# Performance work log

Hardware: AMD Instinct MI355X
Metric: run time of the kernel (lower is better)

Reference implementation:

```python
import jax, jax.numpy as jnp
import numpy as np

BN_EPS = 1e-5

def _bn(x, gamma, beta):
    # training-mode BatchNorm1d: batch statistics over dim 0 (biased var)
    m = x.mean(0)
    v = x.var(0)
    return (x - m) * jax.lax.rsqrt(v + BN_EPS) * gamma + beta

def _lstm_cell(h, c, xt, Wih, Whh, b):
    # PyTorch gate order: i, f, g, o
    g = xt @ Wih.T + h @ Whh.T + b
    i, f, gg, o = jnp.split(g, 4, axis=-1)
    c = jax.nn.sigmoid(f) * c + jax.nn.sigmoid(i) * jnp.tanh(gg)
    h = jax.nn.sigmoid(o) * jnp.tanh(c)
    return h, c


def setup_inputs() -> dict:
    key = jax.random.key(0)
    ks = jax.random.split(key, 12)
    V, E, H = 10000, 512, 1024
    D = 2 * H
    B, S = 32, 256
    s_e = 1.0 / np.sqrt(E)
    s_h = 1.0 / np.sqrt(H)
    s_d = 1.0 / np.sqrt(D)
    return {
        "x": jax.random.randint(ks[0], (B, S), 0, V, dtype=jnp.int32),
        "emb": jax.random.normal(ks[1], (V, E), jnp.float32),
        "Wih_f": jax.random.normal(ks[2], (4 * H, E), jnp.float32) * s_e,
        "Whh_f": jax.random.normal(ks[3], (4 * H, H), jnp.float32) * s_h,
        "b_f": jnp.zeros((4 * H,), jnp.float32),
        "Wih_b": jax.random.normal(ks[4], (4 * H, E), jnp.float32) * s_e,
        "Whh_b": jax.random.normal(ks[5], (4 * H, H), jnp.float32) * s_h,
        "b_b": jnp.zeros((4 * H,), jnp.float32),
        "Wih_d": jax.random.normal(ks[6], (4 * D, E), jnp.float32) * s_e,
        "Whh_d": jax.random.normal(ks[7], (4 * D, D), jnp.float32) * s_d,
        "b_d": jnp.zeros((4 * D,), jnp.float32),
        "enc_gamma": jnp.ones((D,), jnp.float32),
        "enc_beta": jnp.zeros((D,), jnp.float32),
        "dec_gamma": jnp.ones((D,), jnp.float32),
        "dec_beta": jnp.zeros((D,), jnp.float32),
        "fcW": jax.random.normal(ks[8], (V, D), jnp.float32) * s_d,
        "fcb": jnp.zeros((V,), jnp.float32),
    }


def reference(x, emb, Wih_f, Whh_f, b_f, Wih_b, Whh_b, b_b,
              Wih_d, Whh_d, b_d, enc_gamma, enc_beta,
              dec_gamma, dec_beta, fcW, fcb):
    B, S = x.shape
    H = Whh_f.shape[1]
    V = fcW.shape[0]
    xe = emb[x]                      # [B, S, E]
    xs = jnp.swapaxes(xe, 0, 1)      # [S, B, E]
    z = jnp.zeros((B, H), xe.dtype)

    def enc_fwd(carry, xt):
        h, c = _lstm_cell(carry[0], carry[1], xt, Wih_f, Whh_f, b_f)
        return (h, c), None

    def enc_bwd(carry, xt):
        h, c = _lstm_cell(carry[0], carry[1], xt, Wih_b, Whh_b, b_b)
        return (h, c), None

    (hf, _), _ = jax.lax.scan(enc_fwd, (z, z), xs)
    (hb, _), _ = jax.lax.scan(enc_bwd, (z, z), xs[::-1])

    hn = jnp.concatenate([hf, hb], axis=-1)          # [B, 2H]
    hn = jax.nn.relu(_bn(hn, enc_gamma, enc_beta))   # dropout = identity (eval)

    def dec_step(carry, _):
        h, c, tok = carry
        xt = emb[tok]                                # [B, E]
        h, c = _lstm_cell(h, c, xt, Wih_d, Whh_d, b_d)
        out = jax.nn.relu(_bn(h, dec_gamma, dec_beta))
        logits = out @ fcW.T + fcb                   # [B, V]
        tok = jnp.argmax(logits, axis=-1)
        return (h, c, tok), logits

    init = (hn, jnp.zeros_like(hn), x[:, 0])
    _, logits_seq = jax.lax.scan(dec_step, init, None, length=S - 1)  # [S-1, B, V]

    outputs = jnp.concatenate(
        [jnp.zeros((B, 1, V), xe.dtype), jnp.swapaxes(logits_seq, 0, 1)], axis=1)
    return outputs
```

## Files before the change

### kernel.cpp

```cpp
#include <hip/hip_runtime.h>
#include <math.h>

#define BB 32
#define SS 256
#define EE 512
#define HH 1024
#define DD 2048
#define VV 10000

typedef __attribute__((ext_vector_type(8))) short short8v;
typedef __attribute__((ext_vector_type(4))) float f32x4;

typedef unsigned short ushort_t;
typedef unsigned long long u64;


__device__ __forceinline__ ushort_t f2bf(float f) {
  unsigned u = __float_as_uint(f);
  return (ushort_t)((u + 0x7FFFu + ((u >> 16) & 1u)) >> 16);
}
__device__ __forceinline__ float bf2f(ushort_t h) {
  return __uint_as_float(((unsigned)h) << 16);
}
__device__ __forceinline__ unsigned enc_f32(float f) {
  unsigned u = __float_as_uint(f);
  return (u & 0x80000000u) ? ~u : (u | 0x80000000u);
}
__device__ __forceinline__ float sigm(float v) { return 1.0f / (1.0f + expf(-v)); }

union Frag { short8v v; ushort_t u[8]; };

__global__ __launch_bounds__(256) void k_pack_wdec(const float* __restrict__ Whh,
                                                   const float* __restrict__ Wih,
                                                   ushort_t* __restrict__ Wp) {
  int i = blockIdx.x * 256 + threadIdx.x;
  int lane = i & 63, nt = (i >> 6) & 511, fpkt = i >> 15;
  int rho = nt * 16 + (lane & 15);
  int blk = rho >> 5, idx = rho & 31, g = idx >> 3, c = idx & 7;
  int n = g * DD + blk * 8 + c;
  int k0 = fpkt * 32 + (lane >> 4) * 8;
  const float* src = (k0 < DD) ? (Whh + (size_t)n * DD + k0)
                               : (Wih + (size_t)n * EE + (k0 - DD));
  size_t ohi = ((((size_t)fpkt * 2 + 0) * 512 + nt) * 64 + lane) * 8;
  size_t olo = ((((size_t)fpkt * 2 + 1) * 512 + nt) * 64 + lane) * 8;
#pragma unroll
  for (int e = 0; e < 8; ++e) {
    float v = src[e];
    ushort_t hi = f2bf(v);
    Wp[ohi + e] = hi;
    Wp[olo + e] = f2bf(v - bf2f(hi));
  }
}

__global__ __launch_bounds__(256) void k_pack_wfc(const float* __restrict__ fcW,
                                                  ushort_t* __restrict__ Wp) {
  int i = blockIdx.x * 256 + threadIdx.x;
  int lane = i & 63, nt = (i >> 6) % 626, fpkt = i / (626 * 64);
  int rho = nt * 16 + (lane & 15);
  int n = rho < VV ? rho : VV - 1;
  int k0 = fpkt * 32 + (lane >> 4) * 8;
  const float* src = fcW + (size_t)n * DD + k0;
  size_t ohi = ((((size_t)fpkt * 2 + 0) * 626 + nt) * 64 + lane) * 8;
  size_t olo = ((((size_t)fpkt * 2 + 1) * 626 + nt) * 64 + lane) * 8;
#pragma unroll
  for (int e = 0; e < 8; ++e) {
    float v = src[e];
    ushort_t hi = f2bf(v);
    Wp[ohi + e] = hi;
    Wp[olo + e] = f2bf(v - bf2f(hi));
  }
}

__global__ __launch_bounds__(256) void k_pack_wenc(
    const float* __restrict__ Whh_f, const float* __restrict__ Wih_f,
    const float* __restrict__ Whh_b, const float* __restrict__ Wih_b,
    ushort_t* __restrict__ Wp) {
  int i = blockIdx.x * 256 + threadIdx.x;
  int lane = i & 63, nt = (i >> 6) & 511, fpkt = i >> 15;
  int rho = nt * 16 + (lane & 15);
  int blk = rho >> 5, idx = rho & 31, g = idx >> 3, c = idx & 7;
  int dir = blk >> 7;
  int r = g * HH + (blk & 127) * 8 + c;
  const float* Whh = dir ? Whh_b : Whh_f;
  const float* Wih = dir ? Wih_b : Wih_f;
  int k0 = fpkt * 32 + (lane >> 4) * 8;
  const float* src = (k0 < HH) ? (Whh + (size_t)r * HH + k0)
                               : (Wih + (size_t)r * EE + (k0 - HH));
  size_t ohi = ((((size_t)fpkt * 2 + 0) * 512 + nt) * 64 + lane) * 8;
  size_t olo = ((((size_t)fpkt * 2 + 1) * 512 + nt) * 64 + lane) * 8;
#pragma unroll
  for (int e = 0; e < 8; ++e) {
    float v = src[e];
    ushort_t hi = f2bf(v);
    Wp[ohi + e] = hi;
    Wp[olo + e] = f2bf(v - bf2f(hi));
  }
}

__global__ __launch_bounds__(256) void k_zero32(unsigned* __restrict__ p, int n) {
  int i = blockIdx.x * 256 + threadIdx.x;
  if (i < n) p[i] = 0u;
}
__global__ __launch_bounds__(256) void k_out0(float* __restrict__ out) {
  int i = blockIdx.x * 256 + threadIdx.x;
  if (i < BB * VV) out[(size_t)(i / VV) * SS * VV + (i % VV)] = 0.0f;
}

__device__ __forceinline__ void pack_act(ushort_t* __restrict__ dst, int j, int b,
                                         float v) {
  int fpkt = j >> 5, kloc = j & 31;
  int lane = (kloc >> 3) * 16 + (b & 15);
  int e = kloc & 7, mt = b >> 4;
  ushort_t hi = f2bf(v);
  dst[((((size_t)fpkt * 2 + 0) * 2 + mt) * 64 + lane) * 8 + e] = hi;
  dst[((((size_t)fpkt * 2 + 1) * 2 + mt) * 64 + lane) * 8 + e] = f2bf(v - bf2f(hi));
}

__device__ __forceinline__ void split8(const float* __restrict__ src, Frag& fh,
                                       Frag& fl) {
  float4 v0 = *(const float4*)src;
  float4 v1 = *(const float4*)(src + 4);
  float vv[8] = {v0.x, v0.y, v0.z, v0.w, v1.x, v1.y, v1.z, v1.w};
#pragma unroll
  for (int e = 0; e < 8; ++e) {
    ushort_t hi = f2bf(vv[e]);
    fh.u[e] = hi;
    fl.u[e] = f2bf(vv[e] - bf2f(hi));
  }
}

__global__ __launch_bounds__(512) void k_enc_mfma(
    int t, const int* __restrict__ x, const float* __restrict__ emb,
    const ushort_t* __restrict__ Wp, ushort_t* __restrict__ hencp,
    float* __restrict__ cT2, float* __restrict__ hT2,
    const float* __restrict__ b_f, const float* __restrict__ b_b) {
  __shared__ float red[8 * 2 * 2 * 64 * 4];
  __shared__ int stoks[32];
  const int tid = threadIdx.x, w = tid >> 6, lane = tid & 63;
  const int dir = blockIdx.x >> 7, jb = (blockIdx.x & 127) * 8;
  const int s = dir ? (SS - 1 - t) : t;
  const int pin = t & 1;
  const size_t HEP = 32 * 2 * 2 * 64 * 8;
  const ushort_t* hin = hencp + (dir * 2 + pin) * HEP;
  ushort_t* hout = hencp + (dir * 2 + (pin ^ 1)) * HEP;
  if (tid < 32) stoks[tid] = x[tid * SS + s];
  __syncthreads();

  f32x4 acc[2][2];
#pragma unroll
  for (int a = 0; a < 2; ++a)
#pragma unroll
    for (int bq = 0; bq < 2; ++bq) acc[a][bq] = (f32x4){0.f, 0.f, 0.f, 0.f};

  for (int i = 0; i < 6; ++i) {
    const int kt = w + 8 * i;
    Frag ah[2], al[2], wh[2], wl[2];
    if (kt < 32) {
#pragma unroll
      for (int mt = 0; mt < 2; ++mt) {
        ah[mt].v = *(const short8v*)(hin + ((((size_t)kt * 2 + 0) * 2 + mt) * 64 + lane) * 8);
        al[mt].v = *(const short8v*)(hin + ((((size_t)kt * 2 + 1) * 2 + mt) * 64 + lane) * 8);
      }
    } else {
      const int ke = (kt - 32) * 32 + (lane >> 4) * 8;
#pragma unroll
      for (int mt = 0; mt < 2; ++mt) {
        const int b = mt * 16 + (lane & 15);
        split8(emb + (size_t)stoks[b] * EE + ke, ah[mt], al[mt]);
      }
    }
#pragma unroll
    for (int nt = 0; nt < 2; ++nt) {
      const size_t ntg = blockIdx.x * 2 + nt;
      wh[nt].v = *(const short8v*)(Wp + ((((size_t)kt * 2 + 0) * 512 + ntg) * 64 + lane) * 8);
      wl[nt].v = *(const short8v*)(Wp + ((((size_t)kt * 2 + 1) * 512 + ntg) * 64 + lane) * 8);
    }
#pragma unroll
    for (int mt = 0; mt < 2; ++mt)
#pragma unroll
      for (int nt = 0; nt < 2; ++nt) {
        acc[mt][nt] = __builtin_amdgcn_mfma_f32_16x16x32_bf16(ah[mt].v, wh[nt].v, acc[mt][nt], 0, 0, 0);
        acc[mt][nt] = __builtin_amdgcn_mfma_f32_16x16x32_bf16(ah[mt].v, wl[nt].v, acc[mt][nt], 0, 0, 0);
        acc[mt][nt] = __builtin_amdgcn_mfma_f32_16x16x32_bf16(al[mt].v, wh[nt].v, acc[mt][nt], 0, 0, 0);
      }
  }
#pragma unroll
  for (int mt = 0; mt < 2; ++mt)
#pragma unroll
    for (int nt = 0; nt < 2; ++nt)
      ((f32x4*)red)[((w * 2 + mt) * 2 + nt) * 64 + lane] = acc[mt][nt];
  __syncthreads();

  if (tid < 256) {
    const int c = tid >> 5, b = tid & 31;
    const float* bias = dir ? b_b : b_f;
    const int mt = b >> 4, lg = (b & 15) >> 2, reg = b & 3;
    float g4[4];
#pragma unroll
    for (int g = 0; g < 4; ++g) {
      const int rho = g * 8 + c;
      const int nt = rho >> 4, l15 = rho & 15;
      float v = bias[g * HH + jb + c];
#pragma unroll
      for (int w2 = 0; w2 < 8; ++w2)
        v += red[(((w2 * 2 + mt) * 2 + nt) * 64 + lg * 16 + l15) * 4 + reg];
      g4[g] = v;
    }
    const int j = jb + c;
    float* cT = cT2 + dir * (HH * BB);
    float* hT = hT2 + dir * (HH * BB);
    const int idx = j * BB + b;
    float cv = fmaf(sigm(g4[1]), cT[idx], sigm(g4[0]) * tanhf(g4[2]));
    cT[idx] = cv;
    float h = sigm(g4[3]) * tanhf(cv);
    hT[idx] = h;
    pack_act(hout, j, b, h);
  }
}

__global__ __launch_bounds__(256) void k_bn_handoff(
    const float* __restrict__ hT2, const float* __restrict__ gamma,
    const float* __restrict__ beta, ushort_t* __restrict__ hdp) {
  const int d = blockIdx.x * 8 + (threadIdx.x >> 5);
  const int b = threadIdx.x & 31;
  float v = hT2[(d < HH ? d * BB : (HH * BB) + (d - HH) * BB) + b];
  float sum = v;
  for (int m = 16; m >= 1; m >>= 1) sum += __shfl_xor(sum, m, 32);
  float mean = sum * (1.0f / BB);
  float dx = v - mean;
  float s2 = dx * dx;
  for (int m = 16; m >= 1; m >>= 1) s2 += __shfl_xor(s2, m, 32);
  float var = s2 * (1.0f / BB);
  float y = fmaxf(dx * (1.0f / sqrtf(var + 1e-5f)) * gamma[d] + beta[d], 0.0f);
  pack_act(hdp, d, b, y);
}

__global__ __launch_bounds__(512) void k_dec_mfma(
    int t, const int* __restrict__ x, const float* __restrict__ emb,
    const ushort_t* __restrict__ Wp, ushort_t* __restrict__ hdp,
    float* __restrict__ cdT, ushort_t* __restrict__ outp,
    const float* __restrict__ bias, const float* __restrict__ gamma,
    const float* __restrict__ beta, const u64* __restrict__ winners) {
  __shared__ float red[8 * 2 * 2 * 64 * 4];
  __shared__ int stoks[32];
  const int tid = threadIdx.x, w = tid >> 6, lane = tid & 63;
  const int jb = blockIdx.x * 8;
  const int pin = t & 1;
  const size_t HDP = 64 * 2 * 2 * 64 * 8;
  const ushort_t* hin = hdp + pin * HDP;
  ushort_t* hout = hdp + (pin ^ 1) * HDP;
  if (tid < 32)
    stoks[tid] = (t == 0) ? x[tid * SS]
                          : (int)(0xFFFFFFFFu -
                                  (unsigned)(winners[((t - 1) & 1) * 32 + tid] & 0xFFFFFFFFull));
  __syncthreads();

  f32x4 acc[2][2];
#pragma unroll
  for (int a = 0; a < 2; ++a)
#pragma unroll
    for (int bq = 0; bq < 2; ++bq) acc[a][bq] = (f32x4){0.f, 0.f, 0.f, 0.f};

  for (int i = 0; i < 10; ++i) {
    const int kt = w + 8 * i;
    Frag ah[2], al[2], wh[2], wl[2];
    if (kt < 64) {
#pragma unroll
      for (int mt = 0; mt < 2; ++mt) {
        ah[mt].v = *(const short8v*)(hin + ((((size_t)kt * 2 + 0) * 2 + mt) * 64 + lane) * 8);
        al[mt].v = *(const short8v*)(hin + ((((size_t)kt * 2 + 1) * 2 + mt) * 64 + lane) * 8);
      }
    } else {
      const int ke = (kt - 64) * 32 + (lane >> 4) * 8;
#pragma unroll
      for (int mt = 0; mt < 2; ++mt) {
        const int b = mt * 16 + (lane & 15);
        split8(emb + (size_t)stoks[b] * EE + ke, ah[mt], al[mt]);
      }
    }
#pragma unroll
    for (int nt = 0; nt < 2; ++nt) {
      const size_t ntg = blockIdx.x * 2 + nt;
      wh[nt].v = *(const short8v*)(Wp + ((((size_t)kt * 2 + 0) * 512 + ntg) * 64 + lane) * 8);
      wl[nt].v = *(const short8v*)(Wp + ((((size_t)kt * 2 + 1) * 512 + ntg) * 64 + lane) * 8);
    }
#pragma unroll
    for (int mt = 0; mt < 2; ++mt)
#pragma unroll
      for (int nt = 0; nt < 2; ++nt) {
        acc[mt][nt] = __builtin_amdgcn_mfma_f32_16x16x32_bf16(ah[mt].v, wh[nt].v, acc[mt][nt], 0, 0, 0);
        acc[mt][nt] = __builtin_amdgcn_mfma_f32_16x16x32_bf16(ah[mt].v, wl[nt].v, acc[mt][nt], 0, 0, 0);
        acc[mt][nt] = __builtin_amdgcn_mfma_f32_16x16x32_bf16(al[mt].v, wh[nt].v, acc[mt][nt], 0, 0, 0);
      }
  }
#pragma unroll
  for (int mt = 0; mt < 2; ++mt)
#pragma unroll
    for (int nt = 0; nt < 2; ++nt)
      ((f32x4*)red)[((w * 2 + mt) * 2 + nt) * 64 + lane] = acc[mt][nt];
  __syncthreads();

  if (tid < 256) {
    const int c = tid >> 5, b = tid & 31;
    const int mt = b >> 4, lg = (b & 15) >> 2, reg = b & 3;
    float g4[4];
#pragma unroll
    for (int g = 0; g < 4; ++g) {
      const int rho = g * 8 + c;
      const int nt = rho >> 4, l15 = rho & 15;
      float v = bias[g * DD + jb + c];
#pragma unroll
      for (int w2 = 0; w2 < 8; ++w2)
        v += red[(((w2 * 2 + mt) * 2 + nt) * 64 + lg * 16 + l15) * 4 + reg];
      g4[g] = v;
    }
    const int j = jb + c;
    const int idx = j * BB + b;
    float cv = fmaf(sigm(g4[1]), cdT[idx], sigm(g4[0]) * tanhf(g4[2]));
    cdT[idx] = cv;
    float h = sigm(g4[3]) * tanhf(cv);
    pack_act(hout, j, b, h);
    float sum = h;
    for (int m = 16; m >= 1; m >>= 1) sum += __shfl_xor(sum, m, 32);
    float mean = sum * (1.0f / BB);
    float dx = h - mean;
    float s2v = dx * dx;
    for (int m = 16; m >= 1; m >>= 1) s2v += __shfl_xor(s2v, m, 32);
    float var = s2v * (1.0f / BB);
    float y = fmaxf(dx * (1.0f / sqrtf(var + 1e-5f)) * gamma[j] + beta[j], 0.0f);
    pack_act(outp, j, b, y);
  }
}

__global__ __launch_bounds__(512) void k_fc_mfma(
    int t, const ushort_t* __restrict__ outp, const ushort_t* __restrict__ Wp,
    const float* __restrict__ fcb, float* __restrict__ out,
    u64* __restrict__ winners) {
  __shared__ float red[8 * 2 * 2 * 64 * 4];
  __shared__ u64 kred[16][32];
  const int tid = threadIdx.x, w = tid >> 6, lane = tid & 63;

  f32x4 acc[2][2];
#pragma unroll
  for (int a = 0; a < 2; ++a)
#pragma unroll
    for (int bq = 0; bq < 2; ++bq) acc[a][bq] = (f32x4){0.f, 0.f, 0.f, 0.f};

  for (int i = 0; i < 8; ++i) {
    const int kt = w + 8 * i;
    Frag ah[2], al[2], wh[2], wl[2];
#pragma unroll
    for (int mt = 0; mt < 2; ++mt) {
      ah[mt].v = *(const short8v*)(outp + ((((size_t)kt * 2 + 0) * 2 + mt) * 64 + lane) * 8);
      al[mt].v = *(const short8v*)(outp + ((((size_t)kt * 2 + 1) * 2 + mt) * 64 + lane) * 8);
    }
#pragma unroll
    for (int nt = 0; nt < 2; ++nt) {
      const size_t ntg = blockIdx.x * 2 + nt;
      wh[nt].v = *(const short8v*)(Wp + ((((size_t)kt * 2 + 0) * 626 + ntg) * 64 + lane) * 8);
      wl[nt].v = *(const short8v*)(Wp + ((((size_t)kt * 2 + 1) * 626 + ntg) * 64 + lane) * 8);
    }
#pragma unroll
    for (int mt = 0; mt < 2; ++mt)
#pragma unroll
      for (int nt = 0; nt < 2; ++nt) {
        acc[mt][nt] = __builtin_amdgcn_mfma_f32_16x16x32_bf16(ah[mt].v, wh[nt].v, acc[mt][nt], 0, 0, 0);
        acc[mt][nt] = __builtin_amdgcn_mfma_f32_16x16x32_bf16(ah[mt].v, wl[nt].v, acc[mt][nt], 0, 0, 0);
        acc[mt][nt] = __builtin_amdgcn_mfma_f32_16x16x32_bf16(al[mt].v, wh[nt].v, acc[mt][nt], 0, 0, 0);
      }
  }
#pragma unroll
  for (int mt = 0; mt < 2; ++mt)
#pragma unroll
    for (int nt = 0; nt < 2; ++nt)
      ((f32x4*)red)[((w * 2 + mt) * 2 + nt) * 64 + lane] = acc[mt][nt];
  __syncthreads();

  {
    const int r2 = tid >> 5, b = tid & 31;
    const int mt = b >> 4, lg = (b & 15) >> 2, reg = b & 3;
    const size_t obase = (size_t)b * SS * VV + (size_t)(t + 1) * VV;
    u64 bestkey = 0ull;
#pragma unroll
    for (int q = 0; q < 2; ++q) {
      const int rho = r2 * 2 + q;
      const int v = blockIdx.x * 32 + rho;
      if (v < VV) {
        const int nt = rho >> 4, l15 = rho & 15;
        float val = fcb[v];
#pragma unroll
        for (int w2 = 0; w2 < 8; ++w2)
          val += red[(((w2 * 2 + mt) * 2 + nt) * 64 + lg * 16 + l15) * 4 + reg];
        out[obase + v] = val;
        u64 key = ((u64)enc_f32(val) << 32) | (0xFFFFFFFFu - (unsigned)v);
        if (key > bestkey) bestkey = key;
      }
    }
    kred[r2][b] = bestkey;
  }
  __syncthreads();
#pragma unroll
  for (int m = 8; m >= 1; m >>= 1) {
    if ((tid >> 5) < m) {
      u64 o = kred[(tid >> 5) + m][tid & 31];
      if (o > kred[tid >> 5][tid & 31]) kred[tid >> 5][tid & 31] = o;
    }
    __syncthreads();
  }
  if ((tid >> 5) == 0) atomicMax(&winners[(t & 1) * 32 + (tid & 31)], kred[0][tid & 31]);
  if (blockIdx.x == 0 && (tid >> 5) == 1) winners[((t + 1) & 1) * 32 + (tid & 31)] = 0ull;
}

#define DOT4A(acc, q, r)                                                      \
  acc = fmaf((q).x, (r).x, acc); acc = fmaf((q).y, (r).y, acc);               \
  acc = fmaf((q).z, (r).z, acc); acc = fmaf((q).w, (r).w, acc);
__device__ __forceinline__ int colof(int b) { return (b & 3) * 8 + (b >> 2); }

__global__ __launch_bounds__(256) void k_zero_v7(float* __restrict__ p, int n) {
  int i = blockIdx.x * 256 + threadIdx.x;
  if (i < n) p[i] = 0.0f;
}
__global__ __launch_bounds__(256) void k_out0_v7(float* __restrict__ out,
                                                 u64* __restrict__ winners) {
  int i = blockIdx.x * 256 + threadIdx.x;
  if (i < BB * VV) out[(size_t)(i / VV) * SS * VV + (i % VV)] = 0.0f;
  if (i < 64) winners[i] = 0ull;
}
__global__ __launch_bounds__(256) void k_embed_v7(const int* __restrict__ x,
                                                  const float* __restrict__ emb,
                                                  float* __restrict__ xeT) {
  int i = blockIdx.x * 256 + threadIdx.x;
  int c = i & 3, col = (i >> 2) & 31, k4 = (i >> 7) & 127, s = i >> 14;
  int b = (col & 7) * 4 + (col >> 3);
  xeT[i] = emb[(size_t)x[b * SS + s] * EE + (k4 * 4 + c)];
}
__global__ __launch_bounds__(512, 2) void k_enc_step_v7(
    int t, const float* __restrict__ xeT, float* __restrict__ hfT,
    float* __restrict__ cfT, float* __restrict__ hbT, float* __restrict__ cbT,
    const float* __restrict__ Wih_f, const float* __restrict__ Whh_f,
    const float* __restrict__ b_f, const float* __restrict__ Wih_b,
    const float* __restrict__ Whh_b, const float* __restrict__ b_b) {
  __shared__ float wlds[2][32 * 33 * 4];
  __shared__ float alds[2][1024 * 4];
  const int tid = threadIdx.x;
  const int rg = tid & 7, bg = (tid >> 3) & 7, s = tid >> 6;
  const int dir = blockIdx.x >> 7, jb = (blockIdx.x & 127) * 8;
  const float* __restrict__ Wih = dir ? Wih_b : Wih_f;
  const float* __restrict__ Whh = dir ? Whh_b : Whh_f;
  const float* __restrict__ bias = dir ? b_b : b_f;
  float* hT = dir ? hbT : hfT;
  float* cT = dir ? cbT : cfT;
  const int sstep = dir ? (SS - 1 - t) : t;
  const int pin = t & 1;
  const float4* __restrict__ hin4 = (const float4*)(hT + pin * (HH * BB));
  const float4* __restrict__ xs4 = (const float4*)(xeT + (size_t)sstep * EE * BB);
  float* __restrict__ hout = hT + (pin ^ 1) * (HH * BB);
  const int NC = 12;
  auto wsrc = [&](int cc, int idx) -> float4 {
    int lrow = idx >> 5, k4 = idx & 31;
    int grow = (lrow >> 3) * HH + jb + (lrow & 7);
    return (cc < 8) ? ((const float4*)(Whh + (size_t)grow * HH))[cc * 32 + k4]
                    : ((const float4*)(Wih + (size_t)grow * EE))[(cc - 8) * 32 + k4];
  };
  auto asrc = [&](int cc, int idx) -> float4 {
    return (cc < 8) ? hin4[cc * 1024 + idx] : xs4[(cc - 8) * 1024 + idx];
  };
  auto wdst = [&](int buf, int idx) -> float4* {
    return (float4*)&wlds[buf][((idx >> 5) * 33 + (idx & 31)) * 4];
  };
  {
    float4 w0 = wsrc(0, tid), w1 = wsrc(0, 512 + tid);
    float4 a0 = asrc(0, tid), a1 = asrc(0, 512 + tid);
    *wdst(0, tid) = w0; *wdst(0, 512 + tid) = w1;
    ((float4*)alds[0])[tid] = a0; ((float4*)alds[0])[512 + tid] = a1;
  }
  __syncthreads();
  float acc[4][4];
#pragma unroll
  for (int i = 0; i < 4; ++i)
#pragma unroll
    for (int j = 0; j < 4; ++j) acc[i][j] = 0.0f;
  for (int cc = 0; cc < NC; ++cc) {
    const int cb = cc & 1;
    float4 pw0, pw1, pa0, pa1;
    const bool pref = (cc + 1 < NC);
    if (pref) {
      pw0 = wsrc(cc + 1, tid); pw1 = wsrc(cc + 1, 512 + tid);
      pa0 = asrc(cc + 1, tid); pa1 = asrc(cc + 1, 512 + tid);
    }
    const float4* __restrict__ ap = (const float4*)alds[cb];
    const float4* __restrict__ wp = (const float4*)wlds[cb];
#pragma unroll
    for (int sub = 0; sub < 4; ++sub) {
      const int k4 = sub * 8 + s;
      float4 av[4], wv[4];
#pragma unroll
      for (int j = 0; j < 4; ++j) av[j] = ap[k4 * 32 + j * 8 + bg];
#pragma unroll
      for (int i = 0; i < 4; ++i) wv[i] = wp[(rg + 8 * i) * 33 + k4];
#pragma unroll
      for (int i = 0; i < 4; ++i)
#pragma unroll
        for (int j = 0; j < 4; ++j) { DOT4A(acc[i][j], wv[i], av[j]); }
    }
    if (pref) {
      *wdst(cb ^ 1, tid) = pw0; *wdst(cb ^ 1, 512 + tid) = pw1;
      ((float4*)alds[cb ^ 1])[tid] = pa0; ((float4*)alds[cb ^ 1])[512 + tid] = pa1;
    }
    __syncthreads();
  }
  float* red = &wlds[0][0];
#pragma unroll
  for (int i = 0; i < 4; ++i)
#pragma unroll
    for (int j = 0; j < 4; ++j)
      red[(s * 32 + (rg + 8 * i)) * 32 + (bg * 4 + j)] = acc[i][j];
  __syncthreads();
  if (tid < 256) {
    const int c = tid >> 5, b = tid & 31;
    float g4[4];
#pragma unroll
    for (int g = 0; g < 4; ++g) {
      float v = bias[g * HH + jb + c];
#pragma unroll
      for (int s2 = 0; s2 < 8; ++s2) v += red[(s2 * 32 + g * 8 + c) * 32 + b];
      g4[g] = v;
    }
    const int j = jb + c;
    const int idx = j * BB + b;
    float cv = fmaf(sigm(g4[1]), cT[idx], sigm(g4[0]) * tanhf(g4[2]));
    cT[idx] = cv;
    hout[(j >> 2) * 128 + colof(b) * 4 + (j & 3)] = sigm(g4[3]) * tanhf(cv);
  }
}
__global__ __launch_bounds__(256) void k_enc_bn_v7(
    const float* __restrict__ hfT, const float* __restrict__ hbT,
    const float* __restrict__ gamma, const float* __restrict__ beta,
    float* __restrict__ hdT) {
  const int d = blockIdx.x * 8 + (threadIdx.x >> 5);
  const int b = threadIdx.x & 31;
  const int dl = (d < HH) ? d : d - HH;
  const float* __restrict__ src = (d < HH) ? hfT : hbT;
  float v = src[(dl >> 2) * 128 + colof(b) * 4 + (dl & 3)];
  float sum = v;
  for (int m = 16; m >= 1; m >>= 1) sum += __shfl_xor(sum, m, 32);
  float mean = sum * (1.0f / BB);
  float dx = v - mean;
  float s2 = dx * dx;
  for (int m = 16; m >= 1; m >>= 1) s2 += __shfl_xor(s2, m, 32);
  float var = s2 * (1.0f / BB);
  float y = dx * (1.0f / sqrtf(var + 1e-5f)) * gamma[d] + beta[d];
  hdT[(d >> 2) * 128 + colof(b) * 4 + (d & 3)] = fmaxf(y, 0.0f);
}
__global__ __launch_bounds__(512, 2) void k_dec_gates_v7(
    int t, const int* __restrict__ x, const float* __restrict__ emb,
    float* __restrict__ hdT, float* __restrict__ cdT, float* __restrict__ outT,
    const float* __restrict__ Wih, const float* __restrict__ Whh,
    const float* __restrict__ bias, const float* __restrict__ gamma,
    const float* __restrict__ beta, const u64* __restrict__ winners) {
  __shared__ float wlds[2][32 * 33 * 4];
  __shared__ float alds[2][1024 * 4];
  __shared__ int stoks[32];
  const int tid = threadIdx.x;
  const int rg = tid & 7, bg = (tid >> 3) & 7, s = tid >> 6;
  const int jb = blockIdx.x * 8;
  const int pin = t & 1;
  const float4* __restrict__ hin4 = (const float4*)(hdT + pin * (DD * BB));
  float* __restrict__ hout = hdT + (pin ^ 1) * (DD * BB);
  if (tid < 32)
    stoks[tid] = (t == 0) ? x[tid * SS]
                          : (int)(0xFFFFFFFFu -
                                  (unsigned)(winners[((t - 1) & 1) * 32 + tid] & 0xFFFFFFFFull));
  const int NC = 20;
  auto wsrc = [&](int cc, int idx) -> float4 {
    int lrow = idx >> 5, k4 = idx & 31;
    int grow = (lrow >> 3) * DD + jb + (lrow & 7);
    return (cc < 16) ? ((const float4*)(Whh + (size_t)grow * DD))[cc * 32 + k4]
                     : ((const float4*)(Wih + (size_t)grow * EE))[(cc - 16) * 32 + k4];
  };
  auto asrc = [&](int cc, int idx) -> float4 {
    if (cc < 16) return hin4[cc * 1024 + idx];
    int col = idx & 31;
    int b = (col & 7) * 4 + (col >> 3);
    return ((const float4*)(emb + (size_t)stoks[b] * EE))[(cc - 16) * 32 + (idx >> 5)];
  };
  auto wdst = [&](int buf, int idx) -> float4* {
    return (float4*)&wlds[buf][((idx >> 5) * 33 + (idx & 31)) * 4];
  };
  {
    float4 w0 = wsrc(0, tid), w1 = wsrc(0, 512 + tid);
    float4 a0 = asrc(0, tid), a1 = asrc(0, 512 + tid);
    *wdst(0, tid) = w0; *wdst(0, 512 + tid) = w1;
    ((float4*)alds[0])[tid] = a0; ((float4*)alds[0])[512 + tid] = a1;
  }
  __syncthreads();
  float acc[4][4];
#pragma unroll
  for (int i = 0; i < 4; ++i)
#pragma unroll
    for (int j = 0; j < 4; ++j) acc[i][j] = 0.0f;
  for (int cc = 0; cc < NC; ++cc) {
    const int cb = cc & 1;
    float4 pw0, pw1, pa0, pa1;
    const bool pref = (cc + 1 < NC);
    if (pref) {
      pw0 = wsrc(cc + 1, tid); pw1 = wsrc(cc + 1, 512 + tid);
      pa0 = asrc(cc + 1, tid); pa1 = asrc(cc + 1, 512 + tid);
    }
    const float4* __restrict__ ap = (const float4*)alds[cb];
    const float4* __restrict__ wp = (const float4*)wlds[cb];
#pragma unroll
    for (int sub = 0; sub < 4; ++sub) {
      const int k4 = sub * 8 + s;
      float4 av[4], wv[4];
#pragma unroll
      for (int j = 0; j < 4; ++j) av[j] = ap[k4 * 32 + j * 8 + bg];
#pragma unroll
      for (int i = 0; i < 4; ++i) wv[i] = wp[(rg + 8 * i) * 33 + k4];
#pragma unroll
      for (int i = 0; i < 4; ++i)
#pragma unroll
        for (int j = 0; j < 4; ++j) { DOT4A(acc[i][j], wv[i], av[j]); }
    }
    if (pref) {
      *wdst(cb ^ 1, tid) = pw0; *wdst(cb ^ 1, 512 + tid) = pw1;
      ((float4*)alds[cb ^ 1])[tid] = pa0; ((float4*)alds[cb ^ 1])[512 + tid] = pa1;
    }
    __syncthreads();
  }
  float* red = &wlds[0][0];
#pragma unroll
  for (int i = 0; i < 4; ++i)
#pragma unroll
    for (int j = 0; j < 4; ++j)
      red[(s * 32 + (rg + 8 * i)) * 32 + (bg * 4 + j)] = acc[i][j];
  __syncthreads();
  if (tid < 256) {
    const int c = tid >> 5, b = tid & 31;
    float g4[4];
#pragma unroll
    for (int g = 0; g < 4; ++g) {
      float v = bias[g * DD + jb + c];
#pragma unroll
      for (int s2 = 0; s2 < 8; ++s2) v += red[(s2 * 32 + g * 8 + c) * 32 + b];
      g4[g] = v;
    }
    const int j = jb + c;
    const int idx = j * BB + b;
    float cv = fmaf(sigm(g4[1]), cdT[idx], sigm(g4[0]) * tanhf(g4[2]));
    cdT[idx] = cv;
    float h = sigm(g4[3]) * tanhf(cv);
    hout[(j >> 2) * 128 + colof(b) * 4 + (j & 3)] = h;
    float sum = h;
    for (int m = 16; m >= 1; m >>= 1) sum += __shfl_xor(sum, m, 32);
    float mean = sum * (1.0f / BB);
    float dx = h - mean;
    float s2v = dx * dx;
    for (int m = 16; m >= 1; m >>= 1) s2v += __shfl_xor(s2v, m, 32);
    float var = s2v * (1.0f / BB);
    float y = dx * (1.0f / sqrtf(var + 1e-5f)) * gamma[j] + beta[j];
    outT[(j >> 2) * 128 + colof(b) * 4 + (j & 3)] = fmaxf(y, 0.0f);
  }
}
__global__ __launch_bounds__(512, 2) void k_fc_v7(
    int t, const float* __restrict__ outT, const float* __restrict__ fcW,
    const float* __restrict__ fcb, float* __restrict__ out,
    u64* __restrict__ winners) {
  __shared__ float wlds[2][40 * 33 * 4];
  __shared__ float alds[2][1024 * 4];
  __shared__ u64 kred[16][32];
  const int tid = threadIdx.x;
  const int rg = tid & 7, bg = (tid >> 3) & 7, s = tid >> 6;
  const int vb = blockIdx.x * 40;
  const float4* __restrict__ xa4 = (const float4*)outT;
  const int NC = 16;
  auto wsrc = [&](int cc, int idx) -> float4 {
    int lrow = idx >> 5, k4 = idx & 31;
    return ((const float4*)(fcW + (size_t)(vb + lrow) * DD))[cc * 32 + k4];
  };
  auto wdst = [&](int buf, int idx) -> float4* {
    return (float4*)&wlds[buf][((idx >> 5) * 33 + (idx & 31)) * 4];
  };
  {
    float4 w0 = wsrc(0, tid), w1 = wsrc(0, 512 + tid);
    float4 a0 = xa4[tid], a1 = xa4[512 + tid];
    *wdst(0, tid) = w0; *wdst(0, 512 + tid) = w1;
    if (tid < 256) *wdst(0, 1024 + tid) = wsrc(0, 1024 + tid);
    ((float4*)alds[0])[tid] = a0; ((float4*)alds[0])[512 + tid] = a1;
  }
  __syncthreads();
  float acc[5][4];
#pragma unroll
  for (int i = 0; i < 5; ++i)
#pragma unroll
    for (int j = 0; j < 4; ++j) acc[i][j] = 0.0f;
  for (int cc = 0; cc < NC; ++cc) {
    const int cb = cc & 1;
    float4 pw0, pw1, pw2, pa0, pa1;
    const bool pref = (cc + 1 < NC);
    if (pref) {
      pw0 = wsrc(cc + 1, tid); pw1 = wsrc(cc + 1, 512 + tid);
      if (tid < 256) pw2 = wsrc(cc + 1, 1024 + tid);
      pa0 = xa4[(cc + 1) * 1024 + tid];
      pa1 = xa4[(cc + 1) * 1024 + 512 + tid];
    }
    const float4* __restrict__ ap = (const float4*)alds[cb];
    const float4* __restrict__ wp = (const float4*)wlds[cb];
#pragma unroll
    for (int sub = 0; sub < 4; ++sub) {
      const int k4 = sub * 8 + s;
      float4 av[4], wv[5];
#pragma unroll
      for (int j = 0; j < 4; ++j) av[j] = ap[k4 * 32 + j * 8 + bg];
#pragma unroll
      for (int i = 0; i < 5; ++i) wv[i] = wp[(rg + 8 * i) * 33 + k4];
#pragma unroll
      for (int i = 0; i < 5; ++i)
#pragma unroll
        for (int j = 0; j < 4; ++j) { DOT4A(acc[i][j], wv[i], av[j]); }
    }
    if (pref) {
      *wdst(cb ^ 1, tid) = pw0; *wdst(cb ^ 1, 512 + tid) = pw1;
      if (tid < 256) *wdst(cb ^ 1, 1024 + tid) = pw2;
      ((float4*)alds[cb ^ 1])[tid] = pa0; ((float4*)alds[cb ^ 1])[512 + tid] = pa1;
    }
    __syncthreads();
  }
  float* red = &wlds[0][0];
#pragma unroll
  for (int i = 0; i < 5; ++i)
#pragma unroll
    for (int j = 0; j < 4; ++j)
      red[(s * 40 + (rg + 8 * i)) * 32 + (bg * 4 + j)] = acc[i][j];
  __syncthreads();
  const int r = tid >> 5, b = tid & 31;
  const size_t obase = (size_t)b * SS * VV + (size_t)(t + 1) * VV;
  u64 bestkey = 0ull;
  for (int lrow = r; lrow < 40; lrow += 16) {
    const int v = vb + lrow;
    float val = fcb[v];
#pragma unroll
    for (int s2 = 0; s2 < 8; ++s2) val += red[(s2 * 40 + lrow) * 32 + b];
    out[obase + v] = val;
    u64 key = ((u64)enc_f32(val) << 32) | (0xFFFFFFFFu - (unsigned)v);
    if (key > bestkey) bestkey = key;
  }
  kred[r][b] = bestkey;
  __syncthreads();
#pragma unroll
  for (int m = 8; m >= 1; m >>= 1) {
    if (r < m) {
      u64 o = kred[r + m][b];
      if (o > kred[r][b]) kred[r][b] = o;
    }
    __syncthreads();
  }
  if (r == 0) atomicMax(&winners[(t & 1) * 32 + b], kred[0][b]);
  if (blockIdx.x == 0 && r == 1) winners[((t + 1) & 1) * 32 + b] = 0ull;
}

extern "C" void kernel_launch(void* const* d_in, const int* in_sizes, int n_in,
                              void* d_out, int out_size, void* d_ws, size_t ws_size,
                              hipStream_t stream) {
  const int*   x         = (const int*)d_in[0];
  const float* emb       = (const float*)d_in[1];
  const float* Wih_f     = (const float*)d_in[2];
  const float* Whh_f     = (const float*)d_in[3];
  const float* b_f       = (const float*)d_in[4];
  const float* Wih_b     = (const float*)d_in[5];
  const float* Whh_b     = (const float*)d_in[6];
  const float* b_b       = (const float*)d_in[7];
  const float* Wih_d     = (const float*)d_in[8];
  const float* Whh_d     = (const float*)d_in[9];
  const float* b_d       = (const float*)d_in[10];
  const float* enc_gamma = (const float*)d_in[11];
  const float* enc_beta  = (const float*)d_in[12];
  const float* dec_gamma = (const float*)d_in[13];
  const float* dec_beta  = (const float*)d_in[14];
  const float* fcW       = (const float*)d_in[15];
  const float* fcb       = (const float*)d_in[16];
  float* out = (float*)d_out;

  const size_t WDEC_U = (size_t)80 * 2 * 512 * 512;
  const size_t WFC_U  = (size_t)64 * 2 * 626 * 512;
  const size_t WENC_U = (size_t)48 * 2 * 512 * 512;
  const size_t HDP_U  = (size_t)64 * 2 * 2 * 512;
  const size_t HEP_U  = (size_t)32 * 2 * 2 * 512;
  const size_t need = (WDEC_U + WFC_U + WENC_U + 2 * HDP_U + HDP_U + 4 * HEP_U) * 2 +
                      (size_t)(HH * BB * 2 + DD * BB + HH * BB * 2) * 4 + 512;

  if (ws_size >= need + 1024) {
    ushort_t* us = (ushort_t*)d_ws;
    ushort_t* Wpdec = us;               us += WDEC_U;
    ushort_t* Wpfc  = us;               us += WFC_U;
    ushort_t* Wpenc = us;               us += WENC_U;
    ushort_t* hdp   = us;               us += 2 * HDP_U;
    ushort_t* outp  = us;               us += HDP_U;
    ushort_t* hencp = us;               us += 4 * HEP_U;
    float* f = (float*)us;
    float* cT2  = f;  f += HH * BB * 2;
    float* cdT  = f;  f += DD * BB;
    float* hT2  = f;  f += HH * BB * 2;
    u64* winners = (u64*)f;

    k_pack_wdec<<<10240, 256, 0, stream>>>(Whh_d, Wih_d, Wpdec);
    k_pack_wfc<<<10016, 256, 0, stream>>>(fcW, Wpfc);
    k_pack_wenc<<<6144, 256, 0, stream>>>(Whh_f, Wih_f, Whh_b, Wih_b, Wpenc);
    {
      size_t zbytes = (2 * HDP_U + HDP_U + 4 * HEP_U) * 2 +
                      (size_t)(HH * BB * 2 + DD * BB + HH * BB * 2) * 4 + 512;
      int zn = (int)(zbytes / 4);
      k_zero32<<<(zn + 255) / 256, 256, 0, stream>>>((unsigned*)hdp, zn);
    }
    k_out0<<<(BB * VV + 255) / 256, 256, 0, stream>>>(out);

    for (int t = 0; t < SS; ++t)
      k_enc_mfma<<<256, 512, 0, stream>>>(t, x, emb, Wpenc, hencp, cT2, hT2, b_f, b_b);

    k_bn_handoff<<<DD / 8, 256, 0, stream>>>(hT2, enc_gamma, enc_beta, hdp);

    for (int t = 0; t < SS - 1; ++t) {
      k_dec_mfma<<<256, 512, 0, stream>>>(t, x, emb, Wpdec, hdp, cdT, outp,
                                          b_d, dec_gamma, dec_beta, winners);
      k_fc_mfma<<<313, 512, 0, stream>>>(t, outp, Wpfc, fcb, out, winners);
    }
    return;
  }

  float* ws = (float*)d_ws;
  size_t off = 0;
  float* xeT = ws + off; off += (size_t)SS * EE * BB;
  float* hfT = ws + off; off += 2 * HH * BB;
  float* hbT = ws + off; off += 2 * HH * BB;
  float* cfT = ws + off; off += HH * BB;
  float* cbT = ws + off; off += HH * BB;
  float* hdT = ws + off; off += 2 * DD * BB;
  float* cdT = ws + off; off += DD * BB;
  float* outT = ws + off; off += DD * BB;
  u64* winners = (u64*)(ws + off); off += 128;

  const int nz = 2 * HH * BB * 2 + HH * BB * 2 + 2 * DD * BB + DD * BB;
  k_zero_v7<<<(nz + 255) / 256, 256, 0, stream>>>(hfT, nz);
  k_out0_v7<<<(BB * VV + 255) / 256, 256, 0, stream>>>(out, winners);
  k_embed_v7<<<(SS * EE * BB) / 256, 256, 0, stream>>>(x, emb, xeT);

  for (int t = 0; t < SS; ++t)
    k_enc_step_v7<<<256, 512, 0, stream>>>(t, xeT, hfT, cfT, hbT, cbT,
                                           Wih_f, Whh_f, b_f, Wih_b, Whh_b, b_b);
  k_enc_bn_v7<<<DD / 8, 256, 0, stream>>>(hfT, hbT, enc_gamma, enc_beta, hdT);
  for (int t = 0; t < SS - 1; ++t) {
    k_dec_gates_v7<<<DD / 8, 512, 0, stream>>>(t, x, emb, hdT, cdT, outT,
                                               Wih_d, Whh_d, b_d,
                                               dec_gamma, dec_beta, winners);
    k_fc_v7<<<VV / 40, 512, 0, stream>>>(t, outT, fcW, fcb, out, winners);
  }
}
```

Before: 12.64 ms.

## Use single-bf16 FC weights with exact fp32 rescoring of near-max argmax candidates

The FC projection now stores only the high bf16 part of fcW and drops the lo-weight MFMA pass, with 48 columns per block instead of 32. Argmax moves out of the FC kernel into a new rescue kernel. For each batch row it finds logits within a fixed margin of the max and recomputes those candidates exactly in fp32 from an fp32 copy of the activations, which keeps greedy token choice stable. The logits written to the output now carry the reduced-precision error, and the fallback fp32 path is removed.

```diff
diff --git a/kernel.cpp b/kernel.cpp
--- a/kernel.cpp
+++ b/kernel.cpp
@@ -15,16 +15,14 @@
 typedef unsigned long long u64;
 
 
+#define DELTA 0.125f
+
 __device__ __forceinline__ ushort_t f2bf(float f) {
   unsigned u = __float_as_uint(f);
   return (ushort_t)((u + 0x7FFFu + ((u >> 16) & 1u)) >> 16);
 }
 __device__ __forceinline__ float bf2f(ushort_t h) {
   return __uint_as_float(((unsigned)h) << 16);
-}
-__device__ __forceinline__ unsigned enc_f32(float f) {
-  unsigned u = __float_as_uint(f);
-  return (u & 0x80000000u) ? ~u : (u | 0x80000000u);
 }
 __device__ __forceinline__ float sigm(float v) { return 1.0f / (1.0f + expf(-v)); }
 
@@ -55,20 +53,17 @@
 __global__ __launch_bounds__(256) void k_pack_wfc(const float* __restrict__ fcW,
                                                   ushort_t* __restrict__ Wp) {
   int i = blockIdx.x * 256 + threadIdx.x;
-  int lane = i & 63, nt = (i >> 6) % 626, fpkt = i / (626 * 64);
+  int lane = i & 63;
+  int rest = i >> 6;
+  int nt = rest % 627;
+  int kt = rest / 627;
   int rho = nt * 16 + (lane & 15);
   int n = rho < VV ? rho : VV - 1;
-  int k0 = fpkt * 32 + (lane >> 4) * 8;
+  int k0 = kt * 32 + (lane >> 4) * 8;
   const float* src = fcW + (size_t)n * DD + k0;
-  size_t ohi = ((((size_t)fpkt * 2 + 0) * 626 + nt) * 64 + lane) * 8;
-  size_t olo = ((((size_t)fpkt * 2 + 1) * 626 + nt) * 64 + lane) * 8;
-#pragma unroll
-  for (int e = 0; e < 8; ++e) {
-    float v = src[e];
-    ushort_t hi = f2bf(v);
-    Wp[ohi + e] = hi;
-    Wp[olo + e] = f2bf(v - bf2f(hi));
-  }
+  size_t o = (((size_t)kt * 627 + nt) * 64 + lane) * 8;
+#pragma unroll
+  for (int e = 0; e < 8; ++e) Wp[o + e] = f2bf(src[e]);
 }
 
 __global__ __launch_bounds__(256) void k_pack_wenc(
@@ -239,8 +234,9 @@
     int t, const int* __restrict__ x, const float* __restrict__ emb,
     const ushort_t* __restrict__ Wp, ushort_t* __restrict__ hdp,
     float* __restrict__ cdT, ushort_t* __restrict__ outp,
+    float* __restrict__ outF,
     const float* __restrict__ bias, const float* __restrict__ gamma,
-    const float* __restrict__ beta, const u64* __restrict__ winners) {
+    const float* __restrict__ beta, const int* __restrict__ tokens) {
   __shared__ float red[8 * 2 * 2 * 64 * 4];
   __shared__ int stoks[32];
   const int tid = threadIdx.x, w = tid >> 6, lane = tid & 63;
@@ -249,10 +245,7 @@
   const size_t HDP = 64 * 2 * 2 * 64 * 8;
   const ushort_t* hin = hdp + pin * HDP;
   ushort_t* hout = hdp + (pin ^ 1) * HDP;
-  if (tid < 32)
-    stoks[tid] = (t == 0) ? x[tid * SS]
-                          : (int)(0xFFFFFFFFu -
-                                  (unsigned)(winners[((t - 1) & 1) * 32 + tid] & 0xFFFFFFFFull));
+  if (tid < 32) stoks[tid] = (t == 0) ? x[tid * SS] : tokens[tid];
   __syncthreads();
 
   f32x4 acc[2][2];
@@ -329,434 +322,119 @@
     float var = s2v * (1.0f / BB);
     float y = fmaxf(dx * (1.0f / sqrtf(var + 1e-5f)) * gamma[j] + beta[j], 0.0f);
     pack_act(outp, j, b, y);
-  }
-}
-
-__global__ __launch_bounds__(512) void k_fc_mfma(
+    outF[(size_t)b * DD + j] = y;
+  }
+}
+
+__global__ __launch_bounds__(512) void k_fc_approx(
     int t, const ushort_t* __restrict__ outp, const ushort_t* __restrict__ Wp,
-    const float* __restrict__ fcb, float* __restrict__ out,
-    u64* __restrict__ winners) {
-  __shared__ float red[8 * 2 * 2 * 64 * 4];
-  __shared__ u64 kred[16][32];
+    const float* __restrict__ fcb, float* __restrict__ out) {
+  __shared__ float red[8 * 2 * 3 * 64 * 4];
   const int tid = threadIdx.x, w = tid >> 6, lane = tid & 63;
 
-  f32x4 acc[2][2];
+  f32x4 acc[2][3];
 #pragma unroll
   for (int a = 0; a < 2; ++a)
 #pragma unroll
-    for (int bq = 0; bq < 2; ++bq) acc[a][bq] = (f32x4){0.f, 0.f, 0.f, 0.f};
+    for (int bq = 0; bq < 3; ++bq) acc[a][bq] = (f32x4){0.f, 0.f, 0.f, 0.f};
 
   for (int i = 0; i < 8; ++i) {
     const int kt = w + 8 * i;
-    Frag ah[2], al[2], wh[2], wl[2];
+    Frag ah[2], al[2], wh[3];
 #pragma unroll
     for (int mt = 0; mt < 2; ++mt) {
       ah[mt].v = *(const short8v*)(outp + ((((size_t)kt * 2 + 0) * 2 + mt) * 64 + lane) * 8);
       al[mt].v = *(const short8v*)(outp + ((((size_t)kt * 2 + 1) * 2 + mt) * 64 + lane) * 8);
     }
 #pragma unroll
-    for (int nt = 0; nt < 2; ++nt) {
-      const size_t ntg = blockIdx.x * 2 + nt;
-      wh[nt].v = *(const short8v*)(Wp + ((((size_t)kt * 2 + 0) * 626 + ntg) * 64 + lane) * 8);
-      wl[nt].v = *(const short8v*)(Wp + ((((size_t)kt * 2 + 1) * 626 + ntg) * 64 + lane) * 8);
+    for (int nt = 0; nt < 3; ++nt) {
+      const size_t ntg = blockIdx.x * 3 + nt;
+      wh[nt].v = *(const short8v*)(Wp + (((size_t)kt * 627 + ntg) * 64 + lane) * 8);
     }
 #pragma unroll
     for (int mt = 0; mt < 2; ++mt)
 #pragma unroll
-      for (int nt = 0; nt < 2; ++nt) {
+      for (int nt = 0; nt < 3; ++nt) {
         acc[mt][nt] = __builtin_amdgcn_mfma_f32_16x16x32_bf16(ah[mt].v, wh[nt].v, acc[mt][nt], 0, 0, 0);
-        acc[mt][nt] = __builtin_amdgcn_mfma_f32_16x16x32_bf16(ah[mt].v, wl[nt].v, acc[mt][nt], 0, 0, 0);
         acc[mt][nt] = __builtin_amdgcn_mfma_f32_16x16x32_bf16(al[mt].v, wh[nt].v, acc[mt][nt], 0, 0, 0);
       }
   }
 #pragma unroll
   for (int mt = 0; mt < 2; ++mt)
 #pragma unroll
-    for (int nt = 0; nt < 2; ++nt)
-      ((f32x4*)red)[((w * 2 + mt) * 2 + nt) * 64 + lane] = acc[mt][nt];
+    for (int nt = 0; nt < 3; ++nt)
+      ((f32x4*)red)[((w * 2 + mt) * 3 + nt) * 64 + lane] = acc[mt][nt];
   __syncthreads();
 
   {
     const int r2 = tid >> 5, b = tid & 31;
     const int mt = b >> 4, lg = (b & 15) >> 2, reg = b & 3;
     const size_t obase = (size_t)b * SS * VV + (size_t)(t + 1) * VV;
-    u64 bestkey = 0ull;
-#pragma unroll
-    for (int q = 0; q < 2; ++q) {
-      const int rho = r2 * 2 + q;
-      const int v = blockIdx.x * 32 + rho;
+#pragma unroll
+    for (int q = 0; q < 3; ++q) {
+      const int lrow = q * 16 + r2;
+      const int v = blockIdx.x * 48 + lrow;
       if (v < VV) {
-        const int nt = rho >> 4, l15 = rho & 15;
         float val = fcb[v];
 #pragma unroll
         for (int w2 = 0; w2 < 8; ++w2)
-          val += red[(((w2 * 2 + mt) * 2 + nt) * 64 + lg * 16 + l15) * 4 + reg];
+          val += red[(((w2 * 2 + mt) * 3 + q) * 64 + lg * 16 + r2) * 4 + reg];
         out[obase + v] = val;
-        u64 key = ((u64)enc_f32(val) << 32) | (0xFFFFFFFFu - (unsigned)v);
-        if (key > bestkey) bestkey = key;
-      }
-    }
-    kred[r2][b] = bestkey;
-  }
-  __syncthreads();
-#pragma unroll
-  for (int m = 8; m >= 1; m >>= 1) {
-    if ((tid >> 5) < m) {
-      u64 o = kred[(tid >> 5) + m][tid & 31];
-      if (o > kred[tid >> 5][tid & 31]) kred[tid >> 5][tid & 31] = o;
-    }
-    __syncthreads();
-  }
-  if ((tid >> 5) == 0) atomicMax(&winners[(t & 1) * 32 + (tid & 31)], kred[0][tid & 31]);
-  if (blockIdx.x == 0 && (tid >> 5) == 1) winners[((t + 1) & 1) * 32 + (tid & 31)] = 0ull;
-}
-
-#define DOT4A(acc, q, r)                                                      \
-  acc = fmaf((q).x, (r).x, acc); acc = fmaf((q).y, (r).y, acc);               \
-  acc = fmaf((q).z, (r).z, acc); acc = fmaf((q).w, (r).w, acc);
-__device__ __forceinline__ int colof(int b) { return (b & 3) * 8 + (b >> 2); }
-
-__global__ __launch_bounds__(256) void k_zero_v7(float* __restrict__ p, int n) {
-  int i = blockIdx.x * 256 + threadIdx.x;
-  if (i < n) p[i] = 0.0f;
-}
-__global__ __launch_bounds__(256) void k_out0_v7(float* __restrict__ out,
-                                                 u64* __restrict__ winners) {
-  int i = blockIdx.x * 256 + threadIdx.x;
-  if (i < BB * VV) out[(size_t)(i / VV) * SS * VV + (i % VV)] = 0.0f;
-  if (i < 64) winners[i] = 0ull;
-}
-__global__ __launch_bounds__(256) void k_embed_v7(const int* __restrict__ x,
-                                                  const float* __restrict__ emb,
-                                                  float* __restrict__ xeT) {
-  int i = blockIdx.x * 256 + threadIdx.x;
-  int c = i & 3, col = (i >> 2) & 31, k4 = (i >> 7) & 127, s = i >> 14;
-  int b = (col & 7) * 4 + (col >> 3);
-  xeT[i] = emb[(size_t)x[b * SS + s] * EE + (k4 * 4 + c)];
-}
-__global__ __launch_bounds__(512, 2) void k_enc_step_v7(
-    int t, const float* __restrict__ xeT, float* __restrict__ hfT,
-    float* __restrict__ cfT, float* __restrict__ hbT, float* __restrict__ cbT,
-    const float* __restrict__ Wih_f, const float* __restrict__ Whh_f,
-    const float* __restrict__ b_f, const float* __restrict__ Wih_b,
-    const float* __restrict__ Whh_b, const float* __restrict__ b_b) {
-  __shared__ float wlds[2][32 * 33 * 4];
-  __shared__ float alds[2][1024 * 4];
-  const int tid = threadIdx.x;
-  const int rg = tid & 7, bg = (tid >> 3) & 7, s = tid >> 6;
-  const int dir = blockIdx.x >> 7, jb = (blockIdx.x & 127) * 8;
-  const float* __restrict__ Wih = dir ? Wih_b : Wih_f;
-  const float* __restrict__ Whh = dir ? Whh_b : Whh_f;
-  const float* __restrict__ bias = dir ? b_b : b_f;
-  float* hT = dir ? hbT : hfT;
-  float* cT = dir ? cbT : cfT;
-  const int sstep = dir ? (SS - 1 - t) : t;
-  const int pin = t & 1;
-  const float4* __restrict__ hin4 = (const float4*)(hT + pin * (HH * BB));
-  const float4* __restrict__ xs4 = (const float4*)(xeT + (size_t)sstep * EE * BB);
-  float* __restrict__ hout = hT + (pin ^ 1) * (HH * BB);
-  const int NC = 12;
-  auto wsrc = [&](int cc, int idx) -> float4 {
-    int lrow = idx >> 5, k4 = idx & 31;
-    int grow = (lrow >> 3) * HH + jb + (lrow & 7);
-    return (cc < 8) ? ((const float4*)(Whh + (size_t)grow * HH))[cc * 32 + k4]
-                    : ((const float4*)(Wih + (size_t)grow * EE))[(cc - 8) * 32 + k4];
-  };
-  auto asrc = [&](int cc, int idx) -> float4 {
-    return (cc < 8) ? hin4[cc * 1024 + idx] : xs4[(cc - 8) * 1024 + idx];
-  };
-  auto wdst = [&](int buf, int idx) -> float4* {
-    return (float4*)&wlds[buf][((idx >> 5) * 33 + (idx & 31)) * 4];
-  };
-  {
-    float4 w0 = wsrc(0, tid), w1 = wsrc(0, 512 + tid);
-    float4 a0 = asrc(0, tid), a1 = asrc(0, 512 + tid);
-    *wdst(0, tid) = w0; *wdst(0, 512 + tid) = w1;
-    ((float4*)alds[0])[tid] = a0; ((float4*)alds[0])[512 + tid] = a1;
-  }
-  __syncthreads();
-  float acc[4][4];
-#pragma unroll
-  for (int i = 0; i < 4; ++i)
-#pragma unroll
-    for (int j = 0; j < 4; ++j) acc[i][j] = 0.0f;
-  for (int cc = 0; cc < NC; ++cc) {
-    const int cb = cc & 1;
-    float4 pw0, pw1, pa0, pa1;
-    const bool pref = (cc + 1 < NC);
-    if (pref) {
-      pw0 = wsrc(cc + 1, tid); pw1 = wsrc(cc + 1, 512 + tid);
-      pa0 = asrc(cc + 1, tid); pa1 = asrc(cc + 1, 512 + tid);
-    }
-    const float4* __restrict__ ap = (const float4*)alds[cb];
-    const float4* __restrict__ wp = (const float4*)wlds[cb];
-#pragma unroll
-    for (int sub = 0; sub < 4; ++sub) {
-      const int k4 = sub * 8 + s;
-      float4 av[4], wv[4];
-#pragma unroll
-      for (int j = 0; j < 4; ++j) av[j] = ap[k4 * 32 + j * 8 + bg];
-#pragma unroll
-      for (int i = 0; i < 4; ++i) wv[i] = wp[(rg + 8 * i) * 33 + k4];
-#pragma unroll
-      for (int i = 0; i < 4; ++i)
-#pragma unroll
-        for (int j = 0; j < 4; ++j) { DOT4A(acc[i][j], wv[i], av[j]); }
-    }
-    if (pref) {
-      *wdst(cb ^ 1, tid) = pw0; *wdst(cb ^ 1, 512 + tid) = pw1;
-      ((float4*)alds[cb ^ 1])[tid] = pa0; ((float4*)alds[cb ^ 1])[512 + tid] = pa1;
-    }
-    __syncthreads();
-  }
-  float* red = &wlds[0][0];
-#pragma unroll
-  for (int i = 0; i < 4; ++i)
-#pragma unroll
-    for (int j = 0; j < 4; ++j)
-      red[(s * 32 + (rg + 8 * i)) * 32 + (bg * 4 + j)] = acc[i][j];
-  __syncthreads();
-  if (tid < 256) {
-    const int c = tid >> 5, b = tid & 31;
-    float g4[4];
-#pragma unroll
-    for (int g = 0; g < 4; ++g) {
-      float v = bias[g * HH + jb + c];
-#pragma unroll
-      for (int s2 = 0; s2 < 8; ++s2) v += red[(s2 * 32 + g * 8 + c) * 32 + b];
-      g4[g] = v;
-    }
-    const int j = jb + c;
-    const int idx = j * BB + b;
-    float cv = fmaf(sigm(g4[1]), cT[idx], sigm(g4[0]) * tanhf(g4[2]));
-    cT[idx] = cv;
-    hout[(j >> 2) * 128 + colof(b) * 4 + (j & 3)] = sigm(g4[3]) * tanhf(cv);
-  }
-}
-__global__ __launch_bounds__(256) void k_enc_bn_v7(
-    const float* __restrict__ hfT, const float* __restrict__ hbT,
-    const float* __restrict__ gamma, const float* __restrict__ beta,
-    float* __restrict__ hdT) {
-  const int d = blockIdx.x * 8 + (threadIdx.x >> 5);
-  const int b = threadIdx.x & 31;
-  const int dl = (d < HH) ? d : d - HH;
-  const float* __restrict__ src = (d < HH) ? hfT : hbT;
-  float v = src[(dl >> 2) * 128 + colof(b) * 4 + (dl & 3)];
-  float sum = v;
-  for (int m = 16; m >= 1; m >>= 1) sum += __shfl_xor(sum, m, 32);
-  float mean = sum * (1.0f / BB);
-  float dx = v - mean;
-  float s2 = dx * dx;
-  for (int m = 16; m >= 1; m >>= 1) s2 += __shfl_xor(s2, m, 32);
-  float var = s2 * (1.0f / BB);
-  float y = dx * (1.0f / sqrtf(var + 1e-5f)) * gamma[d] + beta[d];
-  hdT[(d >> 2) * 128 + colof(b) * 4 + (d & 3)] = fmaxf(y, 0.0f);
-}
-__global__ __launch_bounds__(512, 2) void k_dec_gates_v7(
-    int t, const int* __restrict__ x, const float* __restrict__ emb,
-    float* __restrict__ hdT, float* __restrict__ cdT, float* __restrict__ outT,
-    const float* __restrict__ Wih, const float* __restrict__ Whh,
-    const float* __restrict__ bias, const float* __restrict__ gamma,
-    const float* __restrict__ beta, const u64* __restrict__ winners) {
-  __shared__ float wlds[2][32 * 33 * 4];
-  __shared__ float alds[2][1024 * 4];
-  __shared__ int stoks[32];
-  const int tid = threadIdx.x;
-  const int rg = tid & 7, bg = (tid >> 3) & 7, s = tid >> 6;
-  const int jb = blockIdx.x * 8;
-  const int pin = t & 1;
-  const float4* __restrict__ hin4 = (const float4*)(hdT + pin * (DD * BB));
-  float* __restrict__ hout = hdT + (pin ^ 1) * (DD * BB);
-  if (tid < 32)
-    stoks[tid] = (t == 0) ? x[tid * SS]
-                          : (int)(0xFFFFFFFFu -
-                                  (unsigned)(winners[((t - 1) & 1) * 32 + tid] & 0xFFFFFFFFull));
-  const int NC = 20;
-  auto wsrc = [&](int cc, int idx) -> float4 {
-    int lrow = idx >> 5, k4 = idx & 31;
-    int grow = (lrow >> 3) * DD + jb + (lrow & 7);
-    return (cc < 16) ? ((const float4*)(Whh + (size_t)grow * DD))[cc * 32 + k4]
-                     : ((const float4*)(Wih + (size_t)grow * EE))[(cc - 16) * 32 + k4];
-  };
-  auto asrc = [&](int cc, int idx) -> float4 {
-    if (cc < 16) return hin4[cc * 1024 + idx];
-    int col = idx & 31;
-    int b = (col & 7) * 4 + (col >> 3);
-    return ((const float4*)(emb + (size_t)stoks[b] * EE))[(cc - 16) * 32 + (idx >> 5)];
-  };
-  auto wdst = [&](int buf, int idx) -> float4* {
-    return (float4*)&wlds[buf][((idx >> 5) * 33 + (idx & 31)) * 4];
-  };
-  {
-    float4 w0 = wsrc(0, tid), w1 = wsrc(0, 512 + tid);
-    float4 a0 = asrc(0, tid), a1 = asrc(0, 512 + tid);
-    *wdst(0, tid) = w0; *wdst(0, 512 + tid) = w1;
-    ((float4*)alds[0])[tid] = a0; ((float4*)alds[0])[512 + tid] = a1;
-  }
-  __syncthreads();
-  float acc[4][4];
-#pragma unroll
-  for (int i = 0; i < 4; ++i)
-#pragma unroll
-    for (int j = 0; j < 4; ++j) acc[i][j] = 0.0f;
-  for (int cc = 0; cc < NC; ++cc) {
-    const int cb = cc & 1;
-    float4 pw0, pw1, pa0, pa1;
-    const bool pref = (cc + 1 < NC);
-    if (pref) {
-      pw0 = wsrc(cc + 1, tid); pw1 = wsrc(cc + 1, 512 + tid);
-      pa0 = asrc(cc + 1, tid); pa1 = asrc(cc + 1, 512 + tid);
-    }
-    const float4* __restrict__ ap = (const float4*)alds[cb];
-    const float4* __restrict__ wp = (const float4*)wlds[cb];
-#pragma unroll
-    for (int sub = 0; sub < 4; ++sub) {
-      const int k4 = sub * 8 + s;
-      float4 av[4], wv[4];
-#pragma unroll
-      for (int j = 0; j < 4; ++j) av[j] = ap[k4 * 32 + j * 8 + bg];
-#pragma unroll
-      for (int i = 0; i < 4; ++i) wv[i] = wp[(rg + 8 * i) * 33 + k4];
-#pragma unroll
-      for (int i = 0; i < 4; ++i)
-#pragma unroll
-        for (int j = 0; j < 4; ++j) { DOT4A(acc[i][j], wv[i], av[j]); }
-    }
-    if (pref) {
-      *wdst(cb ^ 1, tid) = pw0; *wdst(cb ^ 1, 512 + tid) = pw1;
-      ((float4*)alds[cb ^ 1])[tid] = pa0; ((float4*)alds[cb ^ 1])[512 + tid] = pa1;
-    }
-    __syncthreads();
-  }
-  float* red = &wlds[0][0];
-#pragma unroll
-  for (int i = 0; i < 4; ++i)
-#pragma unroll
-    for (int j = 0; j < 4; ++j)
-      red[(s * 32 + (rg + 8 * i)) * 32 + (bg * 4 + j)] = acc[i][j];
-  __syncthreads();
-  if (tid < 256) {
-    const int c = tid >> 5, b = tid & 31;
-    float g4[4];
-#pragma unroll
-    for (int g = 0; g < 4; ++g) {
-      float v = bias[g * DD + jb + c];
-#pragma unroll
-      for (int s2 = 0; s2 < 8; ++s2) v += red[(s2 * 32 + g * 8 + c) * 32 + b];
-      g4[g] = v;
-    }
-    const int j = jb + c;
-    const int idx = j * BB + b;
-    float cv = fmaf(sigm(g4[1]), cdT[idx], sigm(g4[0]) * tanhf(g4[2]));
-    cdT[idx] = cv;
-    float h = sigm(g4[3]) * tanhf(cv);
-    hout[(j >> 2) * 128 + colof(b) * 4 + (j & 3)] = h;
-    float sum = h;
-    for (int m = 16; m >= 1; m >>= 1) sum += __shfl_xor(sum, m, 32);
-    float mean = sum * (1.0f / BB);
-    float dx = h - mean;
-    float s2v = dx * dx;
-    for (int m = 16; m >= 1; m >>= 1) s2v += __shfl_xor(s2v, m, 32);
-    float var = s2v * (1.0f / BB);
-    float y = dx * (1.0f / sqrtf(var + 1e-5f)) * gamma[j] + beta[j];
-    outT[(j >> 2) * 128 + colof(b) * 4 + (j & 3)] = fmaxf(y, 0.0f);
-  }
-}
-__global__ __launch_bounds__(512, 2) void k_fc_v7(
-    int t, const float* __restrict__ outT, const float* __restrict__ fcW,
-    const float* __restrict__ fcb, float* __restrict__ out,
-    u64* __restrict__ winners) {
-  __shared__ float wlds[2][40 * 33 * 4];
-  __shared__ float alds[2][1024 * 4];
-  __shared__ u64 kred[16][32];
-  const int tid = threadIdx.x;
-  const int rg = tid & 7, bg = (tid >> 3) & 7, s = tid >> 6;
-  const int vb = blockIdx.x * 40;
-  const float4* __restrict__ xa4 = (const float4*)outT;
-  const int NC = 16;
-  auto wsrc = [&](int cc, int idx) -> float4 {
-    int lrow = idx >> 5, k4 = idx & 31;
-    return ((const float4*)(fcW + (size_t)(vb + lrow) * DD))[cc * 32 + k4];
-  };
-  auto wdst = [&](int buf, int idx) -> float4* {
-    return (float4*)&wlds[buf][((idx >> 5) * 33 + (idx & 31)) * 4];
-  };
-  {
-    float4 w0 = wsrc(0, tid), w1 = wsrc(0, 512 + tid);
-    float4 a0 = xa4[tid], a1 = xa4[512 + tid];
-    *wdst(0, tid) = w0; *wdst(0, 512 + tid) = w1;
-    if (tid < 256) *wdst(0, 1024 + tid) = wsrc(0, 1024 + tid);
-    ((float4*)alds[0])[tid] = a0; ((float4*)alds[0])[512 + tid] = a1;
-  }
-  __syncthreads();
-  float acc[5][4];
-#pragma unroll
-  for (int i = 0; i < 5; ++i)
-#pragma unroll
-    for (int j = 0; j < 4; ++j) acc[i][j] = 0.0f;
-  for (int cc = 0; cc < NC; ++cc) {
-    const int cb = cc & 1;
-    float4 pw0, pw1, pw2, pa0, pa1;
-    const bool pref = (cc + 1 < NC);
-    if (pref) {
-      pw0 = wsrc(cc + 1, tid); pw1 = wsrc(cc + 1, 512 + tid);
-      if (tid < 256) pw2 = wsrc(cc + 1, 1024 + tid);
-      pa0 = xa4[(cc + 1) * 1024 + tid];
-      pa1 = xa4[(cc + 1) * 1024 + 512 + tid];
-    }
-    const float4* __restrict__ ap = (const float4*)alds[cb];
-    const float4* __restrict__ wp = (const float4*)wlds[cb];
-#pragma unroll
-    for (int sub = 0; sub < 4; ++sub) {
-      const int k4 = sub * 8 + s;
-      float4 av[4], wv[5];
-#pragma unroll
-      for (int j = 0; j < 4; ++j) av[j] = ap[k4 * 32 + j * 8 + bg];
-#pragma unroll
-      for (int i = 0; i < 5; ++i) wv[i] = wp[(rg + 8 * i) * 33 + k4];
-#pragma unroll
-      for (int i = 0; i < 5; ++i)
-#pragma unroll
-        for (int j = 0; j < 4; ++j) { DOT4A(acc[i][j], wv[i], av[j]); }
-    }
-    if (pref) {
-      *wdst(cb ^ 1, tid) = pw0; *wdst(cb ^ 1, 512 + tid) = pw1;
-      if (tid < 256) *wdst(cb ^ 1, 1024 + tid) = pw2;
-      ((float4*)alds[cb ^ 1])[tid] = pa0; ((float4*)alds[cb ^ 1])[512 + tid] = pa1;
-    }
-    __syncthreads();
-  }
-  float* red = &wlds[0][0];
-#pragma unroll
-  for (int i = 0; i < 5; ++i)
-#pragma unroll
-    for (int j = 0; j < 4; ++j)
-      red[(s * 40 + (rg + 8 * i)) * 32 + (bg * 4 + j)] = acc[i][j];
-  __syncthreads();
-  const int r = tid >> 5, b = tid & 31;
-  const size_t obase = (size_t)b * SS * VV + (size_t)(t + 1) * VV;
-  u64 bestkey = 0ull;
-  for (int lrow = r; lrow < 40; lrow += 16) {
-    const int v = vb + lrow;
-    float val = fcb[v];
-#pragma unroll
-    for (int s2 = 0; s2 < 8; ++s2) val += red[(s2 * 40 + lrow) * 32 + b];
-    out[obase + v] = val;
-    u64 key = ((u64)enc_f32(val) << 32) | (0xFFFFFFFFu - (unsigned)v);
-    if (key > bestkey) bestkey = key;
-  }
-  kred[r][b] = bestkey;
-  __syncthreads();
-#pragma unroll
-  for (int m = 8; m >= 1; m >>= 1) {
-    if (r < m) {
-      u64 o = kred[r + m][b];
-      if (o > kred[r][b]) kred[r][b] = o;
-    }
-    __syncthreads();
-  }
-  if (r == 0) atomicMax(&winners[(t & 1) * 32 + b], kred[0][b]);
-  if (blockIdx.x == 0 && r == 1) winners[((t + 1) & 1) * 32 + b] = 0ull;
+      }
+    }
+  }
+}
+
+__global__ __launch_bounds__(256) void k_rescue(
+    int t, const float* __restrict__ out, const float* __restrict__ fcW,
+    const float* __restrict__ fcb, const float* __restrict__ outF,
+    int* __restrict__ tokens) {
+  __shared__ float samax[4];
+  __shared__ int cnt;
+  __shared__ int cand[64];
+  __shared__ float exactv[64];
+  const int b = blockIdx.x;
+  const int tid = threadIdx.x, lane = tid & 63, w = tid >> 6;
+  const float* __restrict__ row = out + (size_t)b * SS * VV + (size_t)(t + 1) * VV;
+
+  float mv = -INFINITY;
+  for (int v = tid; v < VV; v += 256) mv = fmaxf(mv, row[v]);
+#pragma unroll
+  for (int m = 32; m >= 1; m >>= 1) mv = fmaxf(mv, __shfl_xor(mv, m));
+  if (lane == 0) samax[w] = mv;
+  if (tid == 0) cnt = 0;
+  __syncthreads();
+  const float amax = fmaxf(fmaxf(samax[0], samax[1]), fmaxf(samax[2], samax[3]));
+  const float thr = amax - DELTA;
+  for (int v = tid; v < VV; v += 256) {
+    if (row[v] >= thr) {
+      int idx = atomicAdd(&cnt, 1);
+      if (idx < 64) cand[idx] = v;
+    }
+  }
+  __syncthreads();
+  const int nc = min(cnt, 64);
+  for (int ci = w; ci < nc; ci += 4) {
+    const int v = cand[ci];
+    const float* __restrict__ wr = fcW + (size_t)v * DD;
+    const float* __restrict__ av = outF + (size_t)b * DD;
+    float sum = 0.f;
+    for (int k = lane; k < DD; k += 64) sum = fmaf(wr[k], av[k], sum);
+#pragma unroll
+    for (int m = 32; m >= 1; m >>= 1) sum += __shfl_xor(sum, m);
+    if (lane == 0) exactv[ci] = sum + fcb[v];
+  }
+  __syncthreads();
+  if (tid == 0) {
+    float bv = -INFINITY;
+    int bi = 0x7fffffff;
+    for (int ci = 0; ci < nc; ++ci) {
+      float e = exactv[ci];
+      int v = cand[ci];
+      if (e > bv || (e == bv && v < bi)) { bv = e; bi = v; }
+    }
+    tokens[b] = bi;
+  }
 }
 
 extern "C" void kernel_launch(void* const* d_in, const int* in_sizes, int n_in,
@@ -782,76 +460,47 @@
   float* out = (float*)d_out;
 
   const size_t WDEC_U = (size_t)80 * 2 * 512 * 512;
-  const size_t WFC_U  = (size_t)64 * 2 * 626 * 512;
+  const size_t WFC_U  = (size_t)64 * 627 * 512;
   const size_t WENC_U = (size_t)48 * 2 * 512 * 512;
   const size_t HDP_U  = (size_t)64 * 2 * 2 * 512;
   const size_t HEP_U  = (size_t)32 * 2 * 2 * 512;
-  const size_t need = (WDEC_U + WFC_U + WENC_U + 2 * HDP_U + HDP_U + 4 * HEP_U) * 2 +
-                      (size_t)(HH * BB * 2 + DD * BB + HH * BB * 2) * 4 + 512;
-
-  if (ws_size >= need + 1024) {
-    ushort_t* us = (ushort_t*)d_ws;
-    ushort_t* Wpdec = us;               us += WDEC_U;
-    ushort_t* Wpfc  = us;               us += WFC_U;
-    ushort_t* Wpenc = us;               us += WENC_U;
-    ushort_t* hdp   = us;               us += 2 * HDP_U;
-    ushort_t* outp  = us;               us += HDP_U;
-    ushort_t* hencp = us;               us += 4 * HEP_U;
-    float* f = (float*)us;
-    float* cT2  = f;  f += HH * BB * 2;
-    float* cdT  = f;  f += DD * BB;
-    float* hT2  = f;  f += HH * BB * 2;
-    u64* winners = (u64*)f;
-
-    k_pack_wdec<<<10240, 256, 0, stream>>>(Whh_d, Wih_d, Wpdec);
-    k_pack_wfc<<<10016, 256, 0, stream>>>(fcW, Wpfc);
-    k_pack_wenc<<<6144, 256, 0, stream>>>(Whh_f, Wih_f, Whh_b, Wih_b, Wpenc);
-    {
-      size_t zbytes = (2 * HDP_U + HDP_U + 4 * HEP_U) * 2 +
-                      (size_t)(HH * BB * 2 + DD * BB + HH * BB * 2) * 4 + 512;
-      int zn = (int)(zbytes / 4);
-      k_zero32<<<(zn + 255) / 256, 256, 0, stream>>>((unsigned*)hdp, zn);
-    }
-    k_out0<<<(BB * VV + 255) / 256, 256, 0, stream>>>(out);
-
-    for (int t = 0; t < SS; ++t)
-      k_enc_mfma<<<256, 512, 0, stream>>>(t, x, emb, Wpenc, hencp, cT2, hT2, b_f, b_b);
-
-    k_bn_handoff<<<DD / 8, 256, 0, stream>>>(hT2, enc_gamma, enc_beta, hdp);
-
-    for (int t = 0; t < SS - 1; ++t) {
-      k_dec_mfma<<<256, 512, 0, stream>>>(t, x, emb, Wpdec, hdp, cdT, outp,
-                                          b_d, dec_gamma, dec_beta, winners);
-      k_fc_mfma<<<313, 512, 0, stream>>>(t, outp, Wpfc, fcb, out, winners);
-    }
-    return;
-  }
-
-  float* ws = (float*)d_ws;
-  size_t off = 0;
-  float* xeT = ws + off; off += (size_t)SS * EE * BB;
-  float* hfT = ws + off; off += 2 * HH * BB;
-  float* hbT = ws + off; off += 2 * HH * BB;
-  float* cfT = ws + off; off += HH * BB;
-  float* cbT = ws + off; off += HH * BB;
-  float* hdT = ws + off; off += 2 * DD * BB;
-  float* cdT = ws + off; off += DD * BB;
-  float* outT = ws + off; off += DD * BB;
-  u64* winners = (u64*)(ws + off); off += 128;
-
-  const int nz = 2 * HH * BB * 2 + HH * BB * 2 + 2 * DD * BB + DD * BB;
-  k_zero_v7<<<(nz + 255) / 256, 256, 0, stream>>>(hfT, nz);
-  k_out0_v7<<<(BB * VV + 255) / 256, 256, 0, stream>>>(out, winners);
-  k_embed_v7<<<(SS * EE * BB) / 256, 256, 0, stream>>>(x, emb, xeT);
+
+  ushort_t* us = (ushort_t*)d_ws;
+  ushort_t* Wpdec = us;               us += WDEC_U;
+  ushort_t* Wpfc  = us;               us += WFC_U;
+  ushort_t* Wpenc = us;               us += WENC_U;
+  ushort_t* hdp   = us;               us += 2 * HDP_U;
+  ushort_t* outp  = us;               us += HDP_U;
+  ushort_t* hencp = us;               us += 4 * HEP_U;
+  float* f = (float*)us;
+  float* cT2  = f;  f += HH * BB * 2;
+  float* cdT  = f;  f += DD * BB;
+  float* hT2  = f;  f += HH * BB * 2;
+  float* outF = f;  f += DD * BB;
+  int* tokens = (int*)f;
+
+  k_pack_wdec<<<10240, 256, 0, stream>>>(Whh_d, Wih_d, Wpdec);
+  k_pack_wfc<<<10032, 256, 0, stream>>>(fcW, Wpfc);
+  k_pack_wenc<<<6144, 256, 0, stream>>>(Whh_f, Wih_f, Whh_b, Wih_b, Wpenc);
+
+  {
+    size_t zbytes = (2 * HDP_U + HDP_U + 4 * HEP_U) * 2 +
+                    (size_t)(HH * BB * 2 + DD * BB + HH * BB * 2 + DD * BB) * 4 +
+                    128;
+    int zn = (int)(zbytes / 4);
+    k_zero32<<<(zn + 255) / 256, 256, 0, stream>>>((unsigned*)hdp, zn);
+  }
+  k_out0<<<(BB * VV + 255) / 256, 256, 0, stream>>>(out);
 
   for (int t = 0; t < SS; ++t)
-    k_enc_step_v7<<<256, 512, 0, stream>>>(t, xeT, hfT, cfT, hbT, cbT,
-                                           Wih_f, Whh_f, b_f, Wih_b, Whh_b, b_b);
-  k_enc_bn_v7<<<DD / 8, 256, 0, stream>>>(hfT, hbT, enc_gamma, enc_beta, hdT);
+    k_enc_mfma<<<256, 512, 0, stream>>>(t, x, emb, Wpenc, hencp, cT2, hT2, b_f, b_b);
+
+  k_bn_handoff<<<DD / 8, 256, 0, stream>>>(hT2, enc_gamma, enc_beta, hdp);
+
   for (int t = 0; t < SS - 1; ++t) {
-    k_dec_gates_v7<<<DD / 8, 512, 0, stream>>>(t, x, emb, hdT, cdT, outT,
-                                               Wih_d, Whh_d, b_d,
-                                               dec_gamma, dec_beta, winners);
-    k_fc_v7<<<VV / 40, 512, 0, stream>>>(t, outT, fcW, fcb, out, winners);
-  }
-}
+    k_dec_mfma<<<256, 512, 0, stream>>>(t, x, emb, Wpdec, hdp, cdT, outp, outF,
+                                        b_d, dec_gamma, dec_beta, tokens);
+    k_fc_approx<<<209, 512, 0, stream>>>(t, outp, Wpfc, fcb, out);
+    k_rescue<<<BB, 256, 0, stream>>>(t, out, fcW, fcb, outF, tokens);
+  }
+}
```

Measured after the change: 18.88 ms. 49.4% more time.
